# Kernel tuning notes

Hardware: AMD Instinct MI355X
Metric: run time of the kernel (lower is better)

The kernel has to match this reference:

```python
import jax, jax.numpy as jnp
import numpy as np
from jax import lax

Z_MAX = 0.3
WAVELENGTHS = jnp.array([0.65, 0.53, 0.47], jnp.float32)
LUMA = jnp.array([0.299, 0.587, 0.114], jnp.float32)


def conv2d(x, w, b):
    # x: (B,C,H,W), w: (O,I,kh,kw), SAME padding, stride 1
    y = lax.conv_general_dilated(x, w, (1, 1), 'SAME',
                                 dimension_numbers=('NCHW', 'OIHW', 'NCHW'))
    return y + b[None, :, None, None]


def group_norm(x, g, b, eps=1e-5):
    # GroupNorm(num_groups=1): normalize over (C,H,W) per sample
    mu = x.mean(axis=(1, 2, 3), keepdims=True)
    var = ((x - mu) ** 2).mean(axis=(1, 2, 3), keepdims=True)
    xn = (x - mu) * lax.rsqrt(var + eps)
    return xn * g[None, :, None, None] + b[None, :, None, None]


def setup_inputs() -> dict:
    key = jax.random.key(0)
    ks = jax.random.split(key, 16)
    B, C, H, W = 8, 3, 512, 512
    PH, ZH, MH = 16, 16, 32
    s = 0.1
    inp = {
        'x': jax.random.uniform(ks[0], (B, C, H, W), jnp.float32),
        'norm_g': jnp.ones((C,), jnp.float32), 'norm_b': jnp.zeros((C,), jnp.float32),
        'ph_w1': jax.random.normal(ks[1], (PH, C, 3, 3), jnp.float32) * s,
        'ph_b1': jnp.zeros((PH,), jnp.float32),
        'ph_w2': jax.random.normal(ks[2], (C, PH, 3, 3), jnp.float32) * s,
        'ph_b2': jnp.zeros((C,), jnp.float32),
        'z_w1': jax.random.normal(ks[3], (ZH, C, 3, 3), jnp.float32) * s,
        'z_b1': jnp.zeros((ZH,), jnp.float32),
        'z_w2': jax.random.normal(ks[4], (C, ZH, 3, 3), jnp.float32) * s,
        'z_b2': jnp.zeros((C,), jnp.float32),
        'freq_gain': jax.random.normal(ks[5], (C,), jnp.float32) * 0.01,
        'mix_w1': jax.random.normal(ks[6], (MH, C + 2, 3, 3), jnp.float32) * s,
        'mix_b1': jnp.zeros((MH,), jnp.float32),
        'gn1_g': jnp.ones((MH,), jnp.float32), 'gn1_b': jnp.zeros((MH,), jnp.float32),
        'mix_w2': jax.random.normal(ks[7], (MH, MH, 3, 3), jnp.float32) * s,
        'mix_b2': jnp.zeros((MH,), jnp.float32),
        'gn2_g': jnp.ones((MH,), jnp.float32), 'gn2_b': jnp.zeros((MH,), jnp.float32),
        'mix_w3': jax.random.normal(ks[8], (C, MH, 1, 1), jnp.float32) * s,
        'mix_b3': jnp.zeros((C,), jnp.float32),
        'se_w1': jax.random.normal(ks[9], (4, C), jnp.float32) * s,   # mid = max(3//4,4)=4
        'se_b1': jnp.zeros((4,), jnp.float32),
        'se_w2': jax.random.normal(ks[10], (C, 4), jnp.float32) * s,
        'se_b2': jnp.zeros((C,), jnp.float32),
        'alpha': jnp.asarray(0.3, jnp.float32),
    }
    return inp


def reference(x, norm_g, norm_b, ph_w1, ph_b1, ph_w2, ph_b2,
              z_w1, z_b1, z_w2, z_b2, freq_gain,
              mix_w1, mix_b1, gn1_g, gn1_b, mix_w2, mix_b2, gn2_g, gn2_b,
              mix_w3, mix_b3, se_w1, se_b1, se_w2, se_b2, alpha):
    B, C, H, W = x.shape
    # 1) norm
    xn = group_norm(x, norm_g, norm_b)
    # 2) phase prediction (small CNN, phi in [-pi, pi])
    h = jax.nn.silu(conv2d(xn, ph_w1, ph_b1))
    phi = jnp.tanh(conv2d(h, ph_w2, ph_b2)) * jnp.pi
    # 3) per-pixel propagation distance z in [0, z_max]
    hz = jax.nn.silu(conv2d(xn, z_w1, z_b1))
    z = jax.nn.sigmoid(conv2d(hz, z_w2, z_b2)) * Z_MAX
    # 4) complex field U0 = amp * exp(i*phi)  (amp_mode='identity')
    U0 = lax.complex(x * jnp.cos(phi), x * jnp.sin(phi))
    # 5) ASM propagation. kz = 2*pi*sqrt(1/lam^2 - fx^2 - fy^2), per-channel wavelength.
    fy = jnp.fft.fftfreq(H).astype(jnp.float32)
    fx = jnp.fft.fftfreq(W).astype(jnp.float32)
    f2 = fy[:, None] ** 2 + fx[None, :] ** 2                     # (H,W)
    inv_l2 = (1.0 / WAVELENGTHS ** 2)[:, None, None]             # (3,1,1)
    kz = 2.0 * jnp.pi * jnp.sqrt(jnp.maximum(inv_l2 - f2[None], 0.0))  # (3,H,W)
    # spatially varying z: base propagation at mean z + spatial phase correction
    z_mean = z.mean(axis=(2, 3), keepdims=True)                  # (B,3,1,1)
    Uf = jnp.fft.fft2(U0)
    Uf = Uf * (1.0 + freq_gain)[None, :, None, None].astype(Uf.dtype)  # FreqEnhance gain
    hp = kz[None] * z_mean                                       # (B,3,H,W)
    Uz = jnp.fft.ifft2(Uf * lax.complex(jnp.cos(hp), jnp.sin(hp)))
    k0 = (2.0 * jnp.pi / WAVELENGTHS)[None, :, None, None]
    cp = k0 * (z - z_mean)
    Uz = Uz * lax.complex(jnp.cos(cp), jnp.sin(cp))
    # 6) J = |Uz| with clamped sqrt
    J = jnp.sqrt(jnp.maximum(Uz.real ** 2 + Uz.imag ** 2, 1e-12))
    # 7) mix head: [x, J_luma, J_contrast] -> delta
    lw = LUMA[None, :, None, None]
    x_l = (x * lw).sum(axis=1, keepdims=True)
    J_l = (J * lw).sum(axis=1, keepdims=True)
    mix_in = jnp.concatenate([x, J_l, J_l - x_l], axis=1)        # (B,5,H,W)
    d = jax.nn.silu(group_norm(conv2d(mix_in, mix_w1, mix_b1), gn1_g, gn1_b))
    d = jax.nn.silu(group_norm(conv2d(d, mix_w2, mix_b2), gn2_g, gn2_b))
    delta = conv2d(d, mix_w3, mix_b3)                            # (B,3,H,W)
    # 8) SE channel attention
    p = delta.mean(axis=(2, 3))                                  # (B,3)
    wse = jax.nn.sigmoid(jax.nn.silu(p @ se_w1.T + se_b1) @ se_w2.T + se_b2)
    delta = delta * wse[:, :, None, None]
    # 9) residual update
    return x + alpha * delta
```

## Files before the change

kernel.cpp:

```cpp
#include <hip/hip_runtime.h>
#include <hip/hip_bf16.h>
#include <math.h>

#define DINL __device__ __forceinline__

namespace {
constexpr int Bn = 8, Cn = 3, Hn = 512, Wn = 512;
constexpr int HW  = Hn * Wn;
constexpr int CHW = Cn * HW;
constexpr float GEPS = 1e-5f;
constexpr float PIf  = 3.14159265358979323846f;

constexpr size_t OFF_RED = 0;
constexpr size_t OFF_PHI = 512;
constexpr size_t OFF_U   = OFF_PHI + (size_t)Bn * CHW * 2;
constexpr size_t OFF_J   = OFF_U   + (size_t)Bn * CHW * 4;
constexpr size_t OFF_D   = OFF_J   + (size_t)Bn * CHW * 2;
constexpr size_t OFF_Y2  = OFF_D   + (size_t)Bn * CHW * 2;
constexpr size_t OFF_W1B = OFF_Y2  + (size_t)Bn * 32 * HW;
constexpr size_t OFF_W2F = OFF_W1B + 3072 * 2;
constexpr size_t OFF_WH1 = OFF_W2F + 9216;
constexpr size_t OFF_WP2 = OFF_WH1 + 4608 * 2;
constexpr size_t OFF_WZ2 = OFF_WP2 + 4608;
constexpr size_t OFF_PRM = OFF_WZ2 + 4608;
constexpr size_t OFF_PART= OFF_PRM + 160 * 4;
constexpr int PZ = 0;
constexpr int PG1 = 24576;
constexpr int PG2 = 40960;
constexpr int PD  = 57344;
}

typedef __bf16 bfx8 __attribute__((ext_vector_type(8)));
typedef float  fx4  __attribute__((ext_vector_type(4)));
typedef float  fx2  __attribute__((ext_vector_type(2)));

DINL float frcp(float a) { return __builtin_amdgcn_rcpf(a); }
DINL float sigm(float a) { return frcp(1.f + __expf(-a)); }
DINL float siluf(float a) { return a * frcp(1.f + __expf(-a)); }
DINL float ftanh(float a) { return 1.f - 2.f * frcp(1.f + __expf(2.f * a)); }
DINL unsigned short f2bf(float f) {
    unsigned u = __float_as_uint(f);
    return (unsigned short)((u + 0x7FFFu + ((u >> 16) & 1u)) >> 16);
}
DINL float bf2f(unsigned short h) {
    return __uint_as_float(((unsigned)h) << 16);
}
DINL unsigned short t1(float a) { return (unsigned short)(__float_as_uint(a) >> 16); }
DINL unsigned t2(float a, float b) {
    return (__float_as_uint(a) >> 16) | (__float_as_uint(b) & 0xFFFF0000u);
}
DINL unsigned char f2f8(float v) {
    return (unsigned char)(__builtin_amdgcn_cvt_pk_fp8_f32(v, v, 0, false) & 0xFF);
}
DINL unsigned short pk8(float a, float b) {
    return (unsigned short)(__builtin_amdgcn_cvt_pk_fp8_f32(a, b, 0, false) & 0xFFFF);
}
DINL unsigned pk4f8(float a, float b, float c, float d) {
    unsigned u = __builtin_amdgcn_cvt_pk_fp8_f32(a, b, 0, false);
    u = __builtin_amdgcn_cvt_pk_fp8_f32(c, d, u, true);
    return u;
}
template<int SEL>
DINL float f8f(unsigned u) { return __builtin_amdgcn_cvt_f32_fp8(u, SEL); }
DINL unsigned pkh(float a, float b) {
    auto h = __builtin_amdgcn_cvt_pkrtz(a, b);
    unsigned u; __builtin_memcpy(&u, &h, 4); return u;
}
DINL float2 uph(unsigned u) {
    _Float16 h[2]; __builtin_memcpy(h, &u, 4);
    return make_float2((float)h[0], (float)h[1]);
}
DINL unsigned short f2h(float a) {
    _Float16 h = (_Float16)a; unsigned short s; __builtin_memcpy(&s, &h, 2); return s;
}
DINL float h2f(unsigned short s) {
    _Float16 h; __builtin_memcpy(&h, &s, 2); return (float)h;
}

DINL int SW(int e) { return e ^ ((e >> 4) & 7); }

DINL float blockReduceSum(float v) {
    __shared__ float sm[4];
    int lane = threadIdx.x & 63, wid = threadIdx.x >> 6;
    #pragma unroll
    for (int o = 32; o > 0; o >>= 1) v += __shfl_down(v, o, 64);
    __syncthreads();
    if (lane == 0) sm[wid] = v;
    __syncthreads();
    if (wid == 0) {
        float r = (lane < 4) ? sm[lane] : 0.f;
        r += __shfl_down(r, 2, 64);
        r += __shfl_down(r, 1, 64);
        return r;
    }
    return 0.f;
}

DINL void blockReduceSum3(float& a, float& b, float& c) {
    __shared__ float sm3[12];
    int lane = threadIdx.x & 63, wid = threadIdx.x >> 6;
    #pragma unroll
    for (int o = 32; o > 0; o >>= 1) {
        a += __shfl_down(a, o, 64);
        b += __shfl_down(b, o, 64);
        c += __shfl_down(c, o, 64);
    }
    __syncthreads();
    if (lane == 0) { sm3[wid] = a; sm3[4 + wid] = b; sm3[8 + wid] = c; }
    __syncthreads();
    if (threadIdx.x == 0) {
        a = sm3[0] + sm3[1] + sm3[2] + sm3[3];
        b = sm3[4] + sm3[5] + sm3[6] + sm3[7];
        c = sm3[8] + sm3[9] + sm3[10] + sm3[11];
    }
}

__global__ __launch_bounds__(256) void k_red(const float* __restrict__ src,
                                             float* __restrict__ dst)
{
    const float4* s4 = (const float4*)(src + (size_t)blockIdx.x * 1024);
    float4 q = s4[threadIdx.x];
    float r = blockReduceSum(q.x + q.y + q.z + q.w);
    if (threadIdx.x == 0) dst[blockIdx.x] = r;
}

__global__ __launch_bounds__(256) void k_init(
    const float* __restrict__ w1, const float* __restrict__ w2,
    const float* __restrict__ phw1, const float* __restrict__ zw1,
    const float* __restrict__ phw2, const float* __restrict__ zw2,
    const float* __restrict__ g2g, const float* __restrict__ g2b,
    const float* __restrict__ w3,
    unsigned short* __restrict__ w1bf, unsigned char* __restrict__ w2f8,
    unsigned short* __restrict__ wh1, unsigned char* __restrict__ wp2,
    unsigned char* __restrict__ wz2, float* __restrict__ prm,
    const float* __restrict__ x, float* __restrict__ part)
{
    if (blockIdx.x < 36) {
        int i = blockIdx.x * 256 + threadIdx.x;
        if (i < 3072) {
            int o = i / 96, k = i - o * 96;
            int ky = k >> 5, r = k & 31, kx = r >> 3, c = r & 7;
            float v = (kx < 3 && c < 5) ? w1[o * 45 + c * 9 + ky * 3 + kx] : 0.f;
            w1bf[i] = f2bf(v);
        }
        if (i < 9216) {
            int tap = i >> 10, rr = i & 1023, o = rr >> 5, ci = rr & 31;
            w2f8[i] = f2f8(w2[o * 288 + ci * 9 + tap]);
        }
        if (i < 4608) {
            int o = i / 96, k = i - o * 96;
            int ky = k >> 5, r = k & 31, kx = r >> 3, c = r & 7;
            float v = 0.f;
            if (kx < 3 && c < 3)
                v = (o < 16) ? phw1[o * 27 + c * 9 + ky * 3 + kx]
                             : zw1[(o - 16) * 27 + c * 9 + ky * 3 + kx];
            wh1[i] = f2bf(v);
        }
        if (i < 4608) {
            int tap = i / 512, rr = i - tap * 512, n = rr >> 5, k = rr & 31;
            float vp = (n < 3 && k < 16) ? phw2[n * 144 + k * 9 + tap] : 0.f;
            float vz = (n < 3) ? zw2[n * 288 + k * 9 + tap] : 0.f;
            wp2[i] = f2f8(vp);
            wz2[i] = f2f8(vz);
        }
        if (i < 160) {
            if (i < 32) {
                int ch = (i & 1) * 16 + (i >> 1);
                prm[i] = g2g[ch];
            } else if (i < 64) {
                int j = i - 32, ch = (j & 1) * 16 + (j >> 1);
                prm[i] = g2b[ch];
            } else {
                int j = (i - 64) & 31, c = (i - 64) >> 5;
                int ch = (j & 1) * 16 + (j >> 1);
                prm[i] = w3[c * 32 + ch];
            }
        }
        return;
    }
    const int bid = blockIdx.x - 36;
    const int b = bid >> 5, blk = bid & 31;
    const float4* xv = (const float4*)(x + (size_t)b * CHW + (size_t)blk * (CHW / 32));
    float s = 0.f, ss = 0.f;
    for (int i = threadIdx.x; i < (CHW / 32) / 4; i += 256) {
        float4 v = xv[i];
        s  += v.x + v.y + v.z + v.w;
        ss += v.x * v.x + v.y * v.y + v.z * v.z + v.w * v.w;
    }
    float rs = blockReduceSum(s);
    float rss = blockReduceSum(ss);
    if (threadIdx.x == 0) {
        part[PG1 + b * 64 + blk] = rs;
        part[PG1 + b * 64 + 32 + blk] = rss;
    }
}

__global__ __launch_bounds__(256) void k_heads(
    const float* __restrict__ x,
    const float* __restrict__ ng, const float* __restrict__ nb,
    const unsigned short* __restrict__ wh1,
    const float* __restrict__ phb1, const float* __restrict__ zb1,
    const unsigned char* __restrict__ wp2, const unsigned char* __restrict__ wz2,
    const float* __restrict__ phb2, const float* __restrict__ zb2,
    unsigned short* __restrict__ phi, float* __restrict__ part)
{
    const int tx0 = blockIdx.x * 16, ty0 = blockIdx.y * 16, b = blockIdx.z;
    const int local = blockIdx.y * 32 + blockIdx.x;
    const bool edge = (blockIdx.x == 0) || (blockIdx.x == 31) ||
                      (blockIdx.y == 0) || (blockIdx.y == 31);
    __shared__ unsigned short mt8[20 * 21 * 8];
    __shared__ __attribute__((aligned(16))) unsigned char ht8[324 * 48];
    __shared__ float xst[2];
    const int t = threadIdx.x;
    {
        const float* px = part + PG1 + (size_t)b * 64;
        float sv  = (t < 32) ? px[t] : 0.f;
        float ssv = (t >= 32 && t < 64) ? px[t] : 0.f;
        float r0 = blockReduceSum(sv);
        float r1 = blockReduceSum(ssv);
        if (t == 0) { xst[0] = r0; xst[1] = r1; }
        __syncthreads();
    }
    const float mu = xst[0] * (1.f / CHW);
    const float rsv = rsqrtf(xst[1] * (1.f / CHW) - mu * mu + GEPS);
    float sc[3], sh[3];
    #pragma unroll
    for (int c = 0; c < 3; ++c) { sc[c] = rsv * ng[c]; sh[c] = nb[c] - mu * rsv * ng[c]; }
    if (edge) {
        for (int e = t; e < 20 * 21; e += 256) {
            int yy = e / 21, xx = e - yy * 21;
            int gy = ty0 - 2 + yy, gx = tx0 - 2 + xx;
            float v0 = 0, v1 = 0, v2 = 0;
            if (xx < 20 && (unsigned)gy < (unsigned)Hn && (unsigned)gx < (unsigned)Wn) {
                size_t p = (size_t)b * CHW + (size_t)gy * Wn + gx;
                v0 = x[p] * sc[0] + sh[0];
                v1 = x[p + HW] * sc[1] + sh[1];
                v2 = x[p + 2 * HW] * sc[2] + sh[2];
            }
            *(uint4*)(mt8 + e * 8) = make_uint4(t2(v0, v1), (unsigned)t1(v2), 0u, 0u);
        }
    } else {
        for (int e = t; e < 20 * 21; e += 256) {
            int yy = e / 21, xx = e - yy * 21;
            float v0 = 0, v1 = 0, v2 = 0;
            if (xx < 20) {
                size_t p = (size_t)b * CHW + (size_t)(ty0 - 2 + yy) * Wn + (tx0 - 2 + xx);
                v0 = x[p] * sc[0] + sh[0];
                v1 = x[p + HW] * sc[1] + sh[1];
                v2 = x[p + 2 * HW] * sc[2] + sh[2];
            }
            *(uint4*)(mt8 + e * 8) = make_uint4(t2(v0, v1), (unsigned)t1(v2), 0u, 0u);
        }
    }
    const int wv = t >> 6, lane = t & 63, ln = lane & 15, q = lane >> 4;
    bfx8 Bf[3][3];
    #pragma unroll
    for (int ks = 0; ks < 3; ++ks)
        #pragma unroll
        for (int nt = 0; nt < 3; ++nt)
            Bf[ks][nt] = *(const bfx8*)(wh1 + (nt * 16 + ln) * 96 + ks * 32 + q * 8);
    float bph[4], bz0[4], bz1[4];
    #pragma unroll
    for (int r = 0; r < 4; ++r) {
        int ch = q * 4 + r;
        bph[r] = phb1[ch]; bz0[r] = zb1[ch]; bz1[r] = zb1[16 + ch];
    }
    __syncthreads();
    for (int mt = wv; mt < 21; mt += 4) {
        int p = mt * 16 + ln; if (p > 323) p = 323;
        const int hy = p / 18, hx = p - hy * 18;
        fx4 a0 = {0,0,0,0}, a1 = {0,0,0,0}, a2 = {0,0,0,0};
        #pragma unroll
        for (int ks = 0; ks < 3; ++ks) {
            bfx8 A = *(const bfx8*)(mt8 + ((hy + ks) * 21 + hx + q) * 8);
            a0 = __builtin_amdgcn_mfma_f32_16x16x32_bf16(Bf[ks][0], A, a0, 0, 0, 0);
            a1 = __builtin_amdgcn_mfma_f32_16x16x32_bf16(Bf[ks][1], A, a1, 0, 0, 0);
            a2 = __builtin_amdgcn_mfma_f32_16x16x32_bf16(Bf[ks][2], A, a2, 0, 0, 0);
        }
        bool live = true;
        if (edge) {
            const int gy = ty0 - 1 + hy, gx = tx0 - 1 + hx;
            live = (unsigned)gy < (unsigned)Hn && (unsigned)gx < (unsigned)Wn;
        }
        unsigned d0 = pk4f8(siluf(a0[0] + bph[0]), siluf(a0[1] + bph[1]),
                            siluf(a0[2] + bph[2]), siluf(a0[3] + bph[3]));
        unsigned d1 = pk4f8(siluf(a1[0] + bz0[0]), siluf(a1[1] + bz0[1]),
                            siluf(a1[2] + bz0[2]), siluf(a1[3] + bz0[3]));
        unsigned d2 = pk4f8(siluf(a2[0] + bz1[0]), siluf(a2[1] + bz1[1]),
                            siluf(a2[2] + bz1[2]), siluf(a2[3] + bz1[3]));
        if (!live) { d0 = 0u; d1 = 0u; d2 = 0u; }
        unsigned* hp = (unsigned*)(ht8 + p * 48 + q * 4);
        hp[0] = d0; hp[4] = d1; hp[8] = d2;
    }
    __syncthreads();
    fx4 accp[4], accz[4];
    #pragma unroll
    for (int i = 0; i < 4; ++i) { accp[i] = fx4{0,0,0,0}; accz[i] = fx4{0,0,0,0}; }
    #pragma unroll
    for (int tap = 0; tap < 9; ++tap) {
        const int ky = tap / 3, kx = tap - ky * 3;
        long Bp = *(const long*)(wp2 + tap * 512 + ln * 32 + q * 8);
        long Bz = *(const long*)(wz2 + tap * 512 + ln * 32 + q * 8);
        #pragma unroll
        for (int i = 0; i < 4; ++i) {
            const int oy = wv * 4 + i;
            const unsigned char* ap = ht8 + ((oy + ky) * 18 + ln + kx) * 48;
            long Ap = *(const long*)(ap + q * 8);
            long Az = *(const long*)(ap + 16 + q * 8);
            accp[i] = __builtin_amdgcn_mfma_f32_16x16x32_fp8_fp8(Ap, Bp, accp[i], 0, 0, 0);
            accz[i] = __builtin_amdgcn_mfma_f32_16x16x32_fp8_fp8(Az, Bz, accz[i], 0, 0, 0);
        }
    }
    __syncthreads();
    float* phs = (float*)ht8;
    float* zs  = phs + 1024;
    if (ln < 3) {
        #pragma unroll
        for (int i = 0; i < 4; ++i)
            #pragma unroll
            for (int r = 0; r < 4; ++r) {
                int pl = (wv * 4 + i) * 16 + q * 4 + r;
                phs[pl * 4 + ln] = accp[i][r];
                zs [pl * 4 + ln] = accz[i][r];
            }
    }
    asm volatile("" ::: "memory");
    float4 pv = ((const float4*)phs)[t];
    float4 zv = ((const float4*)zs)[t];
    const int gy = ty0 + (t >> 4), gx = tx0 + (t & 15);
    size_t pp = (size_t)b * CHW + (size_t)gy * Wn + gx;
    phi[pp]          = f2h(ftanh(pv.x + phb2[0]) * PIf);
    phi[pp + HW]     = f2h(ftanh(pv.y + phb2[1]) * PIf);
    phi[pp + 2 * HW] = f2h(ftanh(pv.z + phb2[2]) * PIf);
    float z0 = sigm(zv.x + zb2[0]) * 0.3f;
    float z1 = sigm(zv.y + zb2[1]) * 0.3f;
    float z2 = sigm(zv.z + zb2[2]) * 0.3f;
    blockReduceSum3(z0, z1, z2);
    if (t == 0) {
        part[PZ + (size_t)(b * 3 + 0) * 1024 + local] = z0;
        part[PZ + (size_t)(b * 3 + 1) * 1024 + local] = z1;
        part[PZ + (size_t)(b * 3 + 2) * 1024 + local] = z2;
    }
}

template<bool INV>
DINL float2* fft512_wave4(float2* a, float2* b, const float2* tw, int l)
{
    float2* src = a; float2* dst = b;
    int s = 1;
    #pragma unroll
    for (int st = 0; st < 4; ++st) {
        #pragma unroll
        for (int h = 0; h < 2; ++h) {
            const int i = l + h * 64;
            const int q = i & (s - 1);
            const int sm = i - q;
            const int si = SW(i);
            float2 A = src[si], B = src[si + 128], C = src[si + 256], D = src[si + 384];
            float t0x = A.x + C.x, t0y = A.y + C.y;
            float t1x = A.x - C.x, t1y = A.y - C.y;
            float t2x = B.x + D.x, t2y = B.y + D.y;
            float t3x = B.x - D.x, t3y = B.y - D.y;
            float i3x = INV ? -t3y : t3y;
            float i3y = INV ? t3x : -t3x;
            float u0x = t0x + t2x, u0y = t0y + t2y;
            float u2x = t0x - t2x, u2y = t0y - t2y;
            float u1x = t1x + i3x, u1y = t1y + i3y;
            float u3x = t1x - i3x, u3y = t1y - i3y;
            float2 w1 = tw[SW(sm)], w2 = tw[SW(2 * sm)], w3 = tw[SW(3 * sm)];
            float w1y = INV ? -w1.y : w1.y;
            float w2y = INV ? -w2.y : w2.y;
            float w3y = INV ? -w3.y : w3.y;
            const int base = q + 4 * sm;
            dst[SW(base)]         = make_float2(u0x, u0y);
            dst[SW(base + s)]     = make_float2(u1x * w1.x - u1y * w1y, u1x * w1y + u1y * w1.x);
            dst[SW(base + 2 * s)] = make_float2(u2x * w2.x - u2y * w2y, u2x * w2y + u2y * w2.x);
            dst[SW(base + 3 * s)] = make_float2(u3x * w3.x - u3y * w3y, u3x * w3y + u3y * w3.x);
        }
        float2* tmp = src; src = dst; dst = tmp;
        s <<= 2;
        asm volatile("" ::: "memory");
    }
    #pragma unroll
    for (int h = 0; h < 4; ++h) {
        const int j = l + h * 64;
        const int sj = SW(j);
        float2 u = src[sj], v = src[sj + 256];
        dst[sj]       = make_float2(u.x + v.x, u.y + v.y);
        dst[sj + 256] = make_float2(u.x - v.x, u.y - v.y);
    }
    float2* tmp = src; src = dst; dst = tmp;
    asm volatile("" ::: "memory");
    return src;
}

__global__ __launch_bounds__(256) void k_fftA(
    const float* __restrict__ x, const unsigned short* __restrict__ phi,
    unsigned* __restrict__ U)
{
    __shared__ float2 buf[4][2][512];
    __shared__ float2 tw[512];
    const int t = threadIdx.x, wv = t >> 6, l = t & 63;
    #pragma unroll
    for (int i = t; i < 512; i += 256) {
        float s, c; __sincosf(-2.f * PIf * (float)i * (1.f / 512.f), &s, &c);
        tw[SW(i)] = make_float2(c, s);
    }
    __syncthreads();
    const size_t line = (size_t)blockIdx.x * 4 + wv;
    const float* xr = x + line * 512;
    const unsigned short* pr = phi + line * 512;
    float2* A = buf[wv][0];
    float2* B = buf[wv][1];
    #pragma unroll
    for (int i = l; i < 512; i += 64) {
        float s, c; __sincosf(h2f(pr[i]), &s, &c);
        float xv = xr[i];
        A[SW(i)] = make_float2(xv * c, xv * s);
    }
    asm volatile("" ::: "memory");
    float2* res = fft512_wave4<false>(A, B, tw, l);
    unsigned* Ur = U + line * 512;
    #pragma unroll
    for (int i = l; i < 512; i += 64) {
        float2 v = res[SW(i)];
        Ur[i] = pkh(v.x, v.y);
    }
}

__global__ __launch_bounds__(256) void k_transpose(unsigned* __restrict__ U)
{
    const int img = blockIdx.y;
    int rem = blockIdx.x, ti = 0;
    while (rem >= 8 - ti) { rem -= 8 - ti; ++ti; }
    const int tj = ti + rem;
    unsigned* Ub = U + (size_t)img * HW;
    __shared__ unsigned ta[64][65];
    __shared__ unsigned tb[64][65];
    const int t = threadIdx.x;
    const int cc = t & 63, r0 = t >> 6;
    const int ar = ti * 64, ac = tj * 64;
    #pragma unroll
    for (int k = 0; k < 16; ++k) {
        int r = r0 + k * 4;
        ta[r][cc] = Ub[(size_t)(ar + r) * 512 + ac + cc];
    }
    if (ti != tj) {
        #pragma unroll
        for (int k = 0; k < 16; ++k) {
            int r = r0 + k * 4;
            tb[r][cc] = Ub[(size_t)(ac + r) * 512 + ar + cc];
        }
    }
    __syncthreads();
    #pragma unroll
    for (int k = 0; k < 16; ++k) {
        int r = r0 + k * 4;
        Ub[(size_t)(ac + r) * 512 + ar + cc] = ta[cc][r];
    }
    if (ti != tj) {
        #pragma unroll
        for (int k = 0; k < 16; ++k) {
            int r = r0 + k * 4;
            Ub[(size_t)(ar + r) * 512 + ac + cc] = tb[cc][r];
        }
    }
}

__global__ __launch_bounds__(256) void k_fftB(
    unsigned* __restrict__ U, const float* __restrict__ part, const float* __restrict__ fgain)
{
    __shared__ float2 buf[4][2][512];
    __shared__ float2 tw[512];
    __shared__ float zmS;
    const int t = threadIdx.x, wv = t >> 6, l = t & 63;
    #pragma unroll
    for (int i = t; i < 512; i += 256) {
        float s, c; __sincosf(-2.f * PIf * (float)i * (1.f / 512.f), &s, &c);
        tw[SW(i)] = make_float2(c, s);
    }
    const int bc0 = (blockIdx.x * 4) >> 9;
    {
        float4 a4 = ((const float4*)(part + PZ + (size_t)bc0 * 1024))[t];
        float r = blockReduceSum(a4.x + a4.y + a4.z + a4.w);
        if (t == 0) zmS = r * (1.f / HW);
    }
    __syncthreads();
    const int line = blockIdx.x * 4 + wv;
    const int bc = line >> 9;
    const int fw = line & 511;
    const int c = bc % 3;
    unsigned* Ur = U + (size_t)line * 512;
    float2* A = buf[wv][0];
    float2* B = buf[wv][1];
    #pragma unroll
    for (int i = l; i < 512; i += 64) A[SW(i)] = uph(Ur[i]);
    asm volatile("" ::: "memory");
    float2* res = fft512_wave4<false>(A, B, tw, l);
    const float zm   = zmS;
    const float gain = 1.f + fgain[c];
    const float lam  = (c == 0) ? 0.65f : (c == 1) ? 0.53f : 0.47f;
    const float il2  = 1.f / (lam * lam);
    const float fwv  = (float)(fw < 256 ? fw : fw - 512) * (1.f / 512.f);
    const float f2w  = fwv * fwv;
    #pragma unroll
    for (int i = l; i < 512; i += 64) {
        float fh = (float)(i < 256 ? i : i - 512) * (1.f / 512.f);
        float kz = 2.f * PIf * sqrtf(fmaxf(il2 - f2w - fh * fh, 0.f));
        float sn, cs; __sincosf(kz * zm, &sn, &cs);
        const int si = SW(i);
        float2 v = res[si];
        res[si] = make_float2(gain * (v.x * cs - v.y * sn), gain * (v.x * sn + v.y * cs));
    }
    asm volatile("" ::: "memory");
    float2* other = (res == A) ? B : A;
    float2* res2 = fft512_wave4<true>(res, other, tw, l);
    #pragma unroll
    for (int i = l; i < 512; i += 64) {
        float2 v = res2[SW(i)];
        Ur[i] = pkh(v.x * (1.f / 512.f), v.y * (1.f / 512.f));
    }
}

__global__ __launch_bounds__(256) void k_fftC(
    const unsigned* __restrict__ U, unsigned short* __restrict__ J)
{
    __shared__ float2 buf[4][2][512];
    __shared__ float2 tw[512];
    const int t = threadIdx.x, wv = t >> 6, l = t & 63;
    #pragma unroll
    for (int i = t; i < 512; i += 256) {
        float s, c; __sincosf(-2.f * PIf * (float)i * (1.f / 512.f), &s, &c);
        tw[SW(i)] = make_float2(c, s);
    }
    __syncthreads();
    const size_t line = (size_t)blockIdx.x * 4 + wv;
    const unsigned* Ur = U + line * 512;
    float2* A = buf[wv][0];
    float2* B = buf[wv][1];
    #pragma unroll
    for (int i = l; i < 512; i += 64) A[SW(i)] = uph(Ur[i]);
    asm volatile("" ::: "memory");
    float2* res = fft512_wave4<true>(A, B, tw, l);
    unsigned short* Jr = J + line * 512;
    #pragma unroll
    for (int i = l; i < 512; i += 64) {
        float2 v = res[SW(i)];
        float re = v.x * (1.f / 512.f), im = v.y * (1.f / 512.f);
        Jr[i] = f2h(sqrtf(fmaxf(re * re + im * im, 1e-12f)));
    }
}

__global__ __launch_bounds__(256) void k_m1(
    const float* __restrict__ x, const unsigned short* __restrict__ Jb,
    const unsigned short* __restrict__ w1bf, const float* __restrict__ b1,
    float* __restrict__ part)
{
    const int tx0 = blockIdx.x * 16, ty0 = blockIdx.y * 16, b = blockIdx.z;
    const int local = blockIdx.y * 32 + blockIdx.x;
    const bool edge = (blockIdx.x == 0) || (blockIdx.x == 31) ||
                      (blockIdx.y == 0) || (blockIdx.y == 31);
    __shared__ unsigned short mt8[18 * 19 * 8];
    const int t = threadIdx.x;
    for (int e = t; e < 18 * 19; e += 256) {
        int yy = e / 19, xx = e - yy * 19;
        int gy = ty0 - 1 + yy, gx = tx0 - 1 + xx;
        float v0 = 0, v1 = 0, v2 = 0, jl = 0, d5 = 0;
        bool ok = edge ? (xx < 18 && (unsigned)gy < (unsigned)Hn && (unsigned)gx < (unsigned)Wn)
                       : (xx < 18);
        if (ok) {
            size_t p = (size_t)b * CHW + (size_t)gy * Wn + gx;
            v0 = x[p]; v1 = x[p + HW]; v2 = x[p + 2 * HW];
            float j0 = h2f(Jb[p]), j1 = h2f(Jb[p + HW]), j2 = h2f(Jb[p + 2 * HW]);
            float xl = 0.299f * v0 + 0.587f * v1 + 0.114f * v2;
            jl = 0.299f * j0 + 0.587f * j1 + 0.114f * j2;
            d5 = jl - xl;
        }
        *(uint4*)(mt8 + e * 8) = make_uint4(t2(v0, v1), t2(v2, jl), (unsigned)t1(d5), 0u);
    }
    __syncthreads();
    const int wv = t >> 6, lane = t & 63, ln = lane & 15, q = lane >> 4;
    bfx8 Bf[3][2];
    #pragma unroll
    for (int ks = 0; ks < 3; ++ks)
        #pragma unroll
        for (int nt = 0; nt < 2; ++nt)
            Bf[ks][nt] = *(const bfx8*)(w1bf + (nt * 16 + ln) * 96 + ks * 32 + q * 8);
    const float b1v0 = b1[ln], b1v1 = b1[16 + ln];
    float s = 0.f, ss = 0.f;
    #pragma unroll
    for (int i = 0; i < 4; ++i) {
        const int oy = wv * 4 + i;
        fx4 a0 = {0.f, 0.f, 0.f, 0.f}, a1 = {0.f, 0.f, 0.f, 0.f};
        #pragma unroll
        for (int ks = 0; ks < 3; ++ks) {
            bfx8 A = *(const bfx8*)(mt8 + ((oy + ks) * 19 + ln + q) * 8);
            a0 = __builtin_amdgcn_mfma_f32_16x16x32_bf16(A, Bf[ks][0], a0, 0, 0, 0);
            a1 = __builtin_amdgcn_mfma_f32_16x16x32_bf16(A, Bf[ks][1], a1, 0, 0, 0);
        }
        #pragma unroll
        for (int r = 0; r < 4; ++r) {
            float u0 = a0[r] + b1v0, u1 = a1[r] + b1v1;
            s += u0 + u1; ss += u0 * u0 + u1 * u1;
        }
    }
    float rs = blockReduceSum(s);
    float rss = blockReduceSum(ss);
    if (t == 0) {
        part[PG1 + (size_t)b * 1024 + local] = rs;
        part[PG1 + (size_t)(8 + b) * 1024 + local] = rss;
    }
}

__global__ __launch_bounds__(256) void k_m2(
    const float* __restrict__ x, const unsigned short* __restrict__ Jb,
    const unsigned short* __restrict__ w1bf, const float* __restrict__ b1,
    const float* __restrict__ g1g, const float* __restrict__ g1b,
    const unsigned char* __restrict__ w2f8, const float* __restrict__ b2,
    float* __restrict__ part, unsigned char* __restrict__ y2)
{
    const int tx0 = blockIdx.x * 16, ty0 = blockIdx.y * 16, b = blockIdx.z;
    const int local = blockIdx.y * 32 + blockIdx.x;
    const bool edge = (blockIdx.x == 0) || (blockIdx.x == 31) ||
                      (blockIdx.y == 0) || (blockIdx.y == 31);
    __shared__ unsigned short mt8[20 * 21 * 8];
    __shared__ __attribute__((aligned(16))) unsigned char dt2[324 * 40];
    __shared__ float g1s[2];
    const int t = threadIdx.x;
    {
        float4 a4 = ((const float4*)(part + PG1 + (size_t)b * 1024))[t];
        float4 c4 = ((const float4*)(part + PG1 + (size_t)(8 + b) * 1024))[t];
        float r0 = blockReduceSum(a4.x + a4.y + a4.z + a4.w);
        float r1 = blockReduceSum(c4.x + c4.y + c4.z + c4.w);
        if (t == 0) { g1s[0] = r0; g1s[1] = r1; }
        __syncthreads();
    }
    const float mu1 = g1s[0] * (1.f / (32.f * HW));
    const float rs1 = rsqrtf(g1s[1] * (1.f / (32.f * HW)) - mu1 * mu1 + GEPS);
    for (int e = t; e < 20 * 21; e += 256) {
        int yy = e / 21, xx = e - yy * 21;
        int gy = ty0 - 2 + yy, gx = tx0 - 2 + xx;
        float v0 = 0, v1 = 0, v2 = 0, jl = 0, d5 = 0;
        bool ok = edge ? (xx < 20 && (unsigned)gy < (unsigned)Hn && (unsigned)gx < (unsigned)Wn)
                       : (xx < 20);
        if (ok) {
            size_t p = (size_t)b * CHW + (size_t)gy * Wn + gx;
            v0 = x[p]; v1 = x[p + HW]; v2 = x[p + 2 * HW];
            float j0 = h2f(Jb[p]), j1 = h2f(Jb[p + HW]), j2 = h2f(Jb[p + 2 * HW]);
            float xl = 0.299f * v0 + 0.587f * v1 + 0.114f * v2;
            jl = 0.299f * j0 + 0.587f * j1 + 0.114f * j2;
            d5 = jl - xl;
        }
        *(uint4*)(mt8 + e * 8) = make_uint4(t2(v0, v1), t2(v2, jl), (unsigned)t1(d5), 0u);
    }
    const int wv = t >> 6, lane = t & 63, ln = lane & 15, q = lane >> 4;
    float scv[2][4], ofv[2][4];
    #pragma unroll
    for (int g = 0; g < 2; ++g)
        #pragma unroll
        for (int r = 0; r < 4; ++r) {
            int ch = g * 16 + q * 4 + r;
            float sg = rs1 * g1g[ch];
            scv[g][r] = sg;
            ofv[g][r] = (b1[ch] - mu1) * sg + g1b[ch];
        }
    bfx8 Bf[3][2];
    #pragma unroll
    for (int ks = 0; ks < 3; ++ks)
        #pragma unroll
        for (int nt = 0; nt < 2; ++nt)
            Bf[ks][nt] = *(const bfx8*)(w1bf + (nt * 16 + ln) * 96 + ks * 32 + q * 8);
    __syncthreads();
    for (int mt = wv; mt < 21; mt += 4) {
        int p = mt * 16 + ln; if (p > 323) p = 323;
        const int hy = p / 18, hx = p - hy * 18;
        fx4 a0 = {0.f, 0.f, 0.f, 0.f}, a1 = {0.f, 0.f, 0.f, 0.f};
        #pragma unroll
        for (int ks = 0; ks < 3; ++ks) {
            bfx8 A = *(const bfx8*)(mt8 + ((hy + ks) * 21 + hx + q) * 8);
            a0 = __builtin_amdgcn_mfma_f32_16x16x32_bf16(Bf[ks][0], A, a0, 0, 0, 0);
            a1 = __builtin_amdgcn_mfma_f32_16x16x32_bf16(Bf[ks][1], A, a1, 0, 0, 0);
        }
        bool live = true;
        if (edge) {
            const int gy = ty0 - 1 + hy, gx = tx0 - 1 + hx;
            live = (unsigned)gy < (unsigned)Hn && (unsigned)gx < (unsigned)Wn;
        }
        unsigned d0 = pk4f8(siluf(a0[0] * scv[0][0] + ofv[0][0]),
                            siluf(a0[1] * scv[0][1] + ofv[0][1]),
                            siluf(a0[2] * scv[0][2] + ofv[0][2]),
                            siluf(a0[3] * scv[0][3] + ofv[0][3]));
        unsigned d1 = pk4f8(siluf(a1[0] * scv[1][0] + ofv[1][0]),
                            siluf(a1[1] * scv[1][1] + ofv[1][1]),
                            siluf(a1[2] * scv[1][2] + ofv[1][2]),
                            siluf(a1[3] * scv[1][3] + ofv[1][3]));
        if (!live) { d0 = 0u; d1 = 0u; }
        unsigned* dp = (unsigned*)(dt2 + p * 40 + q * 4);
        dp[0] = d0; dp[4] = d1;
    }
    __syncthreads();
    fx4 c2[4][2];
    #pragma unroll
    for (int i = 0; i < 4; ++i)
        #pragma unroll
        for (int nt = 0; nt < 2; ++nt)
            c2[i][nt] = fx4{0.f, 0.f, 0.f, 0.f};
    #pragma unroll
    for (int tap = 0; tap < 9; ++tap) {
        const int ky = tap / 3, kx = tap - ky * 3;
        long B0 = *(const long*)(w2f8 + tap * 1024 + ln * 32 + q * 8);
        long B1 = *(const long*)(w2f8 + tap * 1024 + (16 + ln) * 32 + q * 8);
        #pragma unroll
        for (int i = 0; i < 4; ++i) {
            const int oy = wv * 4 + i;
            long A = *(const long*)(dt2 + ((oy + ky) * 18 + ln + kx) * 40 + q * 8);
            c2[i][0] = __builtin_amdgcn_mfma_f32_16x16x32_fp8_fp8(A, B0, c2[i][0], 0, 0, 0);
            c2[i][1] = __builtin_amdgcn_mfma_f32_16x16x32_fp8_fp8(A, B1, c2[i][1], 0, 0, 0);
        }
    }
    float s = 0.f, ss = 0.f;
    const float b2v0 = b2[ln], b2v1 = b2[16 + ln];
    #pragma unroll
    for (int i = 0; i < 4; ++i) {
        const int gy = ty0 + wv * 4 + i;
        #pragma unroll
        for (int r = 0; r < 4; ++r) {
            const int gx = tx0 + q * 4 + r;
            float a0 = c2[i][0][r] + b2v0;
            float a1 = c2[i][1][r] + b2v1;
            s += a0 + a1; ss += a0 * a0 + a1 * a1;
            size_t off = ((size_t)b * HW + (size_t)gy * Wn + gx) * 32 + ln * 2;
            *(unsigned short*)(y2 + off) = pk8(a0, a1);
        }
    }
    float rsum = blockReduceSum(s);
    float rss = blockReduceSum(ss);
    if (t == 0) {
        part[PG2 + (size_t)b * 1024 + local] = rsum;
        part[PG2 + (size_t)(8 + b) * 1024 + local] = rss;
    }
}

__global__ __launch_bounds__(256) void k_m3(
    const unsigned char* __restrict__ y2,
    const float* __restrict__ prm, const float* __restrict__ b3,
    unsigned short* __restrict__ dl, float* __restrict__ part)
{
    const int t = threadIdx.x;
    const int b = blockIdx.x >> 10;
    __shared__ float g2s[2];
    {
        float4 a4 = ((const float4*)(part + PG2 + (size_t)b * 1024))[t];
        float4 c4 = ((const float4*)(part + PG2 + (size_t)(8 + b) * 1024))[t];
        float r0 = blockReduceSum(a4.x + a4.y + a4.z + a4.w);
        float r1 = blockReduceSum(c4.x + c4.y + c4.z + c4.w);
        if (t == 0) { g2s[0] = r0; g2s[1] = r1; }
        __syncthreads();
    }
    const float mu = g2s[0] * (1.f / (32.f * HW));
    const float rs = rsqrtf(g2s[1] * (1.f / (32.f * HW)) - mu * mu + GEPS);
    int idx = blockIdx.x * 256 + t;
    int pix = idx & (HW - 1);
    const int local = blockIdx.x & 1023;
    const uint4* yp = (const uint4*)(y2 + (size_t)idx * 32);
    uint4 L0 = yp[0], L1 = yp[1];
    unsigned Lw[8] = {L0.x, L0.y, L0.z, L0.w, L1.x, L1.y, L1.z, L1.w};
    float a0 = b3[0], a1 = b3[1], a2 = b3[2];
    #pragma unroll
    for (int w = 0; w < 8; ++w) {
        unsigned u = Lw[w];
#if __has_builtin(__builtin_amdgcn_cvt_pk_f32_fp8)
        fx2 lo = __builtin_amdgcn_cvt_pk_f32_fp8(u, false);
        fx2 hi = __builtin_amdgcn_cvt_pk_f32_fp8(u, true);
        float vv[4] = { lo[0], lo[1], hi[0], hi[1] };
#else
        float vv[4] = { f8f<0>(u), f8f<1>(u), f8f<2>(u), f8f<3>(u) };
#endif
        #pragma unroll
        for (int h = 0; h < 4; ++h) {
            int j = w * 4 + h;
            float dn = (vv[h] - mu) * rs * prm[j] + prm[32 + j];
            float sv = siluf(dn);
            a0 += sv * prm[64 + j]; a1 += sv * prm[96 + j]; a2 += sv * prm[128 + j];
        }
    }
    size_t p = (size_t)b * CHW + pix;
    dl[p] = f2h(a0); dl[p + HW] = f2h(a1); dl[p + 2 * HW] = f2h(a2);
    blockReduceSum3(a0, a1, a2);
    if (t == 0) {
        part[PD + (size_t)(b * 3 + 0) * 1024 + local] = a0;
        part[PD + (size_t)(b * 3 + 1) * 1024 + local] = a1;
        part[PD + (size_t)(b * 3 + 2) * 1024 + local] = a2;
    }
}

__global__ void k_se(float* __restrict__ red,
    const float* __restrict__ w1, const float* __restrict__ b1,
    const float* __restrict__ w2, const float* __restrict__ b2,
    const float* __restrict__ alpha)
{
    int b = threadIdx.x;
    if (b < 8) {
        float p0 = red[72 + b * 3 + 0] * (1.f / HW);
        float p1 = red[72 + b * 3 + 1] * (1.f / HW);
        float p2 = red[72 + b * 3 + 2] * (1.f / HW);
        float h[4];
        #pragma unroll
        for (int j = 0; j < 4; ++j) {
            float a = b1[j] + p0 * w1[j * 3] + p1 * w1[j * 3 + 1] + p2 * w1[j * 3 + 2];
            h[j] = siluf(a);
        }
        float al = alpha[0];
        #pragma unroll
        for (int c = 0; c < 3; ++c) {
            float a = b2[c] + h[0] * w2[c * 4] + h[1] * w2[c * 4 + 1]
                            + h[2] * w2[c * 4 + 2] + h[3] * w2[c * 4 + 3];
            red[96 + b * 3 + c] = al * sigm(a);
        }
    }
}

__global__ __launch_bounds__(256) void k_out(
    const float* __restrict__ x, const unsigned short* __restrict__ dl,
    const float* __restrict__ red, float* __restrict__ out)
{
    int i = blockIdx.x * 256 + threadIdx.x;
    float aw = red[96 + (i >> 16)];
    float4 xv = ((const float4*)x)[i];
    uint2 dv2 = ((const uint2*)dl)[i];
    float2 d01 = uph(dv2.x);
    float2 d23 = uph(dv2.y);
    float4 o;
    o.x = xv.x + aw * d01.x; o.y = xv.y + aw * d01.y;
    o.z = xv.z + aw * d23.x; o.w = xv.w + aw * d23.y;
    ((float4*)out)[i] = o;
}

extern "C" void kernel_launch(void* const* d_in, const int* in_sizes, int n_in,
                              void* d_out, int out_size, void* d_ws, size_t ws_size,
                              hipStream_t stream)
{
    const float* x     = (const float*)d_in[0];
    const float* ng    = (const float*)d_in[1];
    const float* nb    = (const float*)d_in[2];
    const float* ph_w1 = (const float*)d_in[3];
    const float* ph_b1 = (const float*)d_in[4];
    const float* ph_w2 = (const float*)d_in[5];
    const float* ph_b2 = (const float*)d_in[6];
    const float* z_w1  = (const float*)d_in[7];
    const float* z_b1  = (const float*)d_in[8];
    const float* z_w2  = (const float*)d_in[9];
    const float* z_b2  = (const float*)d_in[10];
    const float* fgain = (const float*)d_in[11];
    const float* mw1   = (const float*)d_in[12];
    const float* mb1   = (const float*)d_in[13];
    const float* g1g   = (const float*)d_in[14];
    const float* g1b   = (const float*)d_in[15];
    const float* mw2   = (const float*)d_in[16];
    const float* mb2   = (const float*)d_in[17];
    const float* g2g   = (const float*)d_in[18];
    const float* g2b   = (const float*)d_in[19];
    const float* mw3   = (const float*)d_in[20];
    const float* mb3   = (const float*)d_in[21];
    const float* sw1   = (const float*)d_in[22];
    const float* sb1   = (const float*)d_in[23];
    const float* sw2   = (const float*)d_in[24];
    const float* sb2   = (const float*)d_in[25];
    const float* alpha = (const float*)d_in[26];

    char* ws = (char*)d_ws;
    float*  red = (float*)(ws + OFF_RED);
    unsigned short* phi = (unsigned short*)(ws + OFF_PHI);
    unsigned* U = (unsigned*)(ws + OFF_U);
    unsigned short* Jb = (unsigned short*)(ws + OFF_J);
    unsigned short* dl = (unsigned short*)(ws + OFF_D);
    unsigned char*  y2   = (unsigned char*)(ws + OFF_Y2);
    unsigned short* w1bf = (unsigned short*)(ws + OFF_W1B);
    unsigned char*  w2f8 = (unsigned char*)(ws + OFF_W2F);
    unsigned short* wh1  = (unsigned short*)(ws + OFF_WH1);
    unsigned char*  wp2  = (unsigned char*)(ws + OFF_WP2);
    unsigned char*  wz2  = (unsigned char*)(ws + OFF_WZ2);
    float* prm  = (float*)(ws + OFF_PRM);
    float* part = (float*)(ws + OFF_PART);
    float* out = (float*)d_out;

    hipLaunchKernelGGL(k_init, dim3(292), dim3(256), 0, stream,
                       mw1, mw2, ph_w1, z_w1, ph_w2, z_w2, g2g, g2b, mw3,
                       w1bf, w2f8, wh1, wp2, wz2, prm, x, part);
    hipLaunchKernelGGL(k_heads, dim3(32, 32, 8), dim3(256), 0, stream,
                       x, ng, nb, wh1, ph_b1, z_b1, wp2, wz2, ph_b2, z_b2, phi, part);
    hipLaunchKernelGGL(k_fftA, dim3(3072), dim3(256), 0, stream, x, phi, U);
    hipLaunchKernelGGL(k_transpose, dim3(36, 24), dim3(256), 0, stream, U);
    hipLaunchKernelGGL(k_fftB, dim3(3072), dim3(256), 0, stream, U, part, fgain);
    hipLaunchKernelGGL(k_transpose, dim3(36, 24), dim3(256), 0, stream, U);
    hipLaunchKernelGGL(k_fftC, dim3(3072), dim3(256), 0, stream, U, Jb);
    hipLaunchKernelGGL(k_m1, dim3(32, 32, 8), dim3(256), 0, stream, x, Jb, w1bf, mb1, part);
    hipLaunchKernelGGL(k_m2, dim3(32, 32, 8), dim3(256), 0, stream,
                       x, Jb, w1bf, mb1, g1g, g1b, w2f8, mb2, part, y2);
    hipLaunchKernelGGL(k_m3, dim3(8192), dim3(256), 0, stream, y2, prm, mb3, dl, part);
    hipLaunchKernelGGL(k_red, dim3(24), dim3(256), 0, stream, part + PD, red + 72);
    hipLaunchKernelGGL(k_se, dim3(1), dim3(64), 0, stream, red, sw1, sb1, sw2, sb2, alpha);
    hipLaunchKernelGGL(k_out, dim3(6144), dim3(256), 0, stream, x, dl, red, out);
}
```

Before: 466.0 us.

## Precompute FFT twiddles, LUT-based GN2+SiLU in m3, merge final reductions

FFT twiddles are computed once in k_init into a global table, and the FFT kernels load them instead of calling sincos per block. The z-mean reduction moves from every k_fftB block into one transpose block per image. k_m3 now handles 2048 pixels per block and builds an 8192-entry shared-memory table of normalized SiLU values indexed by fp8 code, replacing per-element conversion and exp. k_red and k_se are merged into a single k_fin launch. The table build costs extra setup per block, and the larger blocks reduce parallelism in k_m3.

```diff
diff --git a/kernel.cpp b/kernel.cpp
--- a/kernel.cpp
+++ b/kernel.cpp
@@ -24,6 +24,7 @@
 constexpr size_t OFF_WZ2 = OFF_WP2 + 4608;
 constexpr size_t OFF_PRM = OFF_WZ2 + 4608;
 constexpr size_t OFF_PART= OFF_PRM + 160 * 4;
+constexpr size_t OFF_TW  = OFF_PART + 81920 * 4;
 constexpr int PZ = 0;
 constexpr int PG1 = 24576;
 constexpr int PG2 = 40960;
@@ -113,15 +114,6 @@
         b = sm3[4] + sm3[5] + sm3[6] + sm3[7];
         c = sm3[8] + sm3[9] + sm3[10] + sm3[11];
     }
-}
-
-__global__ __launch_bounds__(256) void k_red(const float* __restrict__ src,
-                                             float* __restrict__ dst)
-{
-    const float4* s4 = (const float4*)(src + (size_t)blockIdx.x * 1024);
-    float4 q = s4[threadIdx.x];
-    float r = blockReduceSum(q.x + q.y + q.z + q.w);
-    if (threadIdx.x == 0) dst[blockIdx.x] = r;
 }
 
 __global__ __launch_bounds__(256) void k_init(
@@ -133,6 +125,7 @@
     unsigned short* __restrict__ w1bf, unsigned char* __restrict__ w2f8,
     unsigned short* __restrict__ wh1, unsigned char* __restrict__ wp2,
     unsigned char* __restrict__ wz2, float* __restrict__ prm,
+    float2* __restrict__ gtw,
     const float* __restrict__ x, float* __restrict__ part)
 {
     if (blockIdx.x < 36) {
@@ -178,7 +171,14 @@
         }
         return;
     }
-    const int bid = blockIdx.x - 36;
+    if (blockIdx.x == 36) {
+        for (int i = threadIdx.x; i < 512; i += 256) {
+            float s, c; __sincosf(-2.f * PIf * (float)i * (1.f / 512.f), &s, &c);
+            gtw[i] = make_float2(c, s);
+        }
+        return;
+    }
+    const int bid = blockIdx.x - 37;
     const int b = bid >> 5, blk = bid & 31;
     const float4* xv = (const float4*)(x + (size_t)b * CHW + (size_t)blk * (CHW / 32));
     float s = 0.f, ss = 0.f;
@@ -396,16 +396,13 @@
 
 __global__ __launch_bounds__(256) void k_fftA(
     const float* __restrict__ x, const unsigned short* __restrict__ phi,
-    unsigned* __restrict__ U)
+    unsigned* __restrict__ U, const float2* __restrict__ gtw)
 {
     __shared__ float2 buf[4][2][512];
     __shared__ float2 tw[512];
     const int t = threadIdx.x, wv = t >> 6, l = t & 63;
     #pragma unroll
-    for (int i = t; i < 512; i += 256) {
-        float s, c; __sincosf(-2.f * PIf * (float)i * (1.f / 512.f), &s, &c);
-        tw[SW(i)] = make_float2(c, s);
-    }
+    for (int i = t; i < 512; i += 256) tw[SW(i)] = gtw[i];
     __syncthreads();
     const size_t line = (size_t)blockIdx.x * 4 + wv;
     const float* xr = x + line * 512;
@@ -428,9 +425,16 @@
     }
 }
 
-__global__ __launch_bounds__(256) void k_transpose(unsigned* __restrict__ U)
+__global__ __launch_bounds__(256) void k_transpose(unsigned* __restrict__ U,
+                                                   const float* __restrict__ part,
+                                                   float* __restrict__ red)
 {
     const int img = blockIdx.y;
+    if (blockIdx.x == 0) {
+        float4 a4 = ((const float4*)(part + PZ + (size_t)img * 1024))[threadIdx.x];
+        float r = blockReduceSum(a4.x + a4.y + a4.z + a4.w);
+        if (threadIdx.x == 0) red[16 + img] = r;
+    }
     int rem = blockIdx.x, ti = 0;
     while (rem >= 8 - ti) { rem -= 8 - ti; ++ti; }
     const int tj = ti + rem;
@@ -468,28 +472,20 @@
 }
 
 __global__ __launch_bounds__(256) void k_fftB(
-    unsigned* __restrict__ U, const float* __restrict__ part, const float* __restrict__ fgain)
+    unsigned* __restrict__ U, const float* __restrict__ red,
+    const float* __restrict__ fgain, const float2* __restrict__ gtw)
 {
     __shared__ float2 buf[4][2][512];
     __shared__ float2 tw[512];
-    __shared__ float zmS;
     const int t = threadIdx.x, wv = t >> 6, l = t & 63;
     #pragma unroll
-    for (int i = t; i < 512; i += 256) {
-        float s, c; __sincosf(-2.f * PIf * (float)i * (1.f / 512.f), &s, &c);
-        tw[SW(i)] = make_float2(c, s);
-    }
-    const int bc0 = (blockIdx.x * 4) >> 9;
-    {
-        float4 a4 = ((const float4*)(part + PZ + (size_t)bc0 * 1024))[t];
-        float r = blockReduceSum(a4.x + a4.y + a4.z + a4.w);
-        if (t == 0) zmS = r * (1.f / HW);
-    }
-    __syncthreads();
+    for (int i = t; i < 512; i += 256) tw[SW(i)] = gtw[i];
     const int line = blockIdx.x * 4 + wv;
     const int bc = line >> 9;
     const int fw = line & 511;
     const int c = bc % 3;
+    const float zm = red[16 + bc] * (1.f / HW);
+    __syncthreads();
     unsigned* Ur = U + (size_t)line * 512;
     float2* A = buf[wv][0];
     float2* B = buf[wv][1];
@@ -497,7 +493,6 @@
     for (int i = l; i < 512; i += 64) A[SW(i)] = uph(Ur[i]);
     asm volatile("" ::: "memory");
     float2* res = fft512_wave4<false>(A, B, tw, l);
-    const float zm   = zmS;
     const float gain = 1.f + fgain[c];
     const float lam  = (c == 0) ? 0.65f : (c == 1) ? 0.53f : 0.47f;
     const float il2  = 1.f / (lam * lam);
@@ -523,16 +518,14 @@
 }
 
 __global__ __launch_bounds__(256) void k_fftC(
-    const unsigned* __restrict__ U, unsigned short* __restrict__ J)
+    const unsigned* __restrict__ U, unsigned short* __restrict__ J,
+    const float2* __restrict__ gtw)
 {
     __shared__ float2 buf[4][2][512];
     __shared__ float2 tw[512];
     const int t = threadIdx.x, wv = t >> 6, l = t & 63;
     #pragma unroll
-    for (int i = t; i < 512; i += 256) {
-        float s, c; __sincosf(-2.f * PIf * (float)i * (1.f / 512.f), &s, &c);
-        tw[SW(i)] = make_float2(c, s);
-    }
+    for (int i = t; i < 512; i += 256) tw[SW(i)] = gtw[i];
     __syncthreads();
     const size_t line = (size_t)blockIdx.x * 4 + wv;
     const unsigned* Ur = U + line * 512;
@@ -747,8 +740,10 @@
     unsigned short* __restrict__ dl, float* __restrict__ part)
 {
     const int t = threadIdx.x;
-    const int b = blockIdx.x >> 10;
+    const int b = blockIdx.x >> 7;
+    const int local = blockIdx.x & 127;
     __shared__ float g2s[2];
+    __shared__ float lut[8192];
     {
         float4 a4 = ((const float4*)(part + PG2 + (size_t)b * 1024))[t];
         float4 c4 = ((const float4*)(part + PG2 + (size_t)(8 + b) * 1024))[t];
@@ -759,51 +754,66 @@
     }
     const float mu = g2s[0] * (1.f / (32.f * HW));
     const float rs = rsqrtf(g2s[1] * (1.f / (32.f * HW)) - mu * mu + GEPS);
-    int idx = blockIdx.x * 256 + t;
-    int pix = idx & (HW - 1);
-    const int local = blockIdx.x & 1023;
-    const uint4* yp = (const uint4*)(y2 + (size_t)idx * 32);
-    uint4 L0 = yp[0], L1 = yp[1];
-    unsigned Lw[8] = {L0.x, L0.y, L0.z, L0.w, L1.x, L1.y, L1.z, L1.w};
-    float a0 = b3[0], a1 = b3[1], a2 = b3[2];
-    #pragma unroll
-    for (int w = 0; w < 8; ++w) {
-        unsigned u = Lw[w];
-#if __has_builtin(__builtin_amdgcn_cvt_pk_f32_fp8)
-        fx2 lo = __builtin_amdgcn_cvt_pk_f32_fp8(u, false);
-        fx2 hi = __builtin_amdgcn_cvt_pk_f32_fp8(u, true);
-        float vv[4] = { lo[0], lo[1], hi[0], hi[1] };
-#else
-        float vv[4] = { f8f<0>(u), f8f<1>(u), f8f<2>(u), f8f<3>(u) };
-#endif
-        #pragma unroll
-        for (int h = 0; h < 4; ++h) {
-            int j = w * 4 + h;
-            float dn = (vv[h] - mu) * rs * prm[j] + prm[32 + j];
-            float sv = siluf(dn);
-            a0 += sv * prm[64 + j]; a1 += sv * prm[96 + j]; a2 += sv * prm[128 + j];
-        }
-    }
-    size_t p = (size_t)b * CHW + pix;
-    dl[p] = f2h(a0); dl[p + HW] = f2h(a1); dl[p + 2 * HW] = f2h(a2);
-    blockReduceSum3(a0, a1, a2);
+    for (int e = t; e < 8192; e += 256) {
+        int j = e >> 8;
+        float v = f8f<0>((unsigned)(e & 255));
+        lut[e] = siluf((v - mu) * rs * prm[j] + prm[32 + j]);
+    }
+    __syncthreads();
+    const float bb0 = b3[0], bb1 = b3[1], bb2 = b3[2];
+    float s0 = 0.f, s1 = 0.f, s2 = 0.f;
+    #pragma unroll
+    for (int k = 0; k < 8; ++k) {
+        int idx = blockIdx.x * 2048 + k * 256 + t;
+        int pix = idx & (HW - 1);
+        const uint4* yp = (const uint4*)(y2 + (size_t)idx * 32);
+        uint4 L0 = yp[0], L1 = yp[1];
+        unsigned Lw[8] = {L0.x, L0.y, L0.z, L0.w, L1.x, L1.y, L1.z, L1.w};
+        float a0 = bb0, a1 = bb1, a2 = bb2;
+        #pragma unroll
+        for (int w = 0; w < 8; ++w) {
+            unsigned u = Lw[w];
+            #pragma unroll
+            for (int h = 0; h < 4; ++h) {
+                int j = w * 4 + h;
+                int code = (int)((u >> (8 * h)) & 255u);
+                float sv = lut[j * 256 + code];
+                a0 += sv * prm[64 + j]; a1 += sv * prm[96 + j]; a2 += sv * prm[128 + j];
+            }
+        }
+        size_t p = (size_t)b * CHW + pix;
+        dl[p] = f2h(a0); dl[p + HW] = f2h(a1); dl[p + 2 * HW] = f2h(a2);
+        s0 += a0; s1 += a1; s2 += a2;
+    }
+    blockReduceSum3(s0, s1, s2);
     if (t == 0) {
-        part[PD + (size_t)(b * 3 + 0) * 1024 + local] = a0;
-        part[PD + (size_t)(b * 3 + 1) * 1024 + local] = a1;
-        part[PD + (size_t)(b * 3 + 2) * 1024 + local] = a2;
-    }
-}
-
-__global__ void k_se(float* __restrict__ red,
+        part[PD + (size_t)(b * 3 + 0) * 1024 + local] = s0;
+        part[PD + (size_t)(b * 3 + 1) * 1024 + local] = s1;
+        part[PD + (size_t)(b * 3 + 2) * 1024 + local] = s2;
+    }
+}
+
+__global__ __launch_bounds__(256) void k_fin(
+    const float* __restrict__ part, float* __restrict__ red,
     const float* __restrict__ w1, const float* __restrict__ b1,
     const float* __restrict__ w2, const float* __restrict__ b2,
     const float* __restrict__ alpha)
 {
-    int b = threadIdx.x;
-    if (b < 8) {
-        float p0 = red[72 + b * 3 + 0] * (1.f / HW);
-        float p1 = red[72 + b * 3 + 1] * (1.f / HW);
-        float p2 = red[72 + b * 3 + 2] * (1.f / HW);
+    __shared__ float sm[24];
+    const int t = threadIdx.x, wv = t >> 6, l = t & 63;
+    for (int g = wv; g < 24; g += 4) {
+        const float* p = part + PD + (size_t)g * 1024;
+        float s = p[l] + p[l + 64];
+        #pragma unroll
+        for (int o = 32; o > 0; o >>= 1) s += __shfl_down(s, o, 64);
+        if (l == 0) sm[g] = s;
+    }
+    __syncthreads();
+    if (t < 8) {
+        int b = t;
+        float p0 = sm[b * 3 + 0] * (1.f / HW);
+        float p1 = sm[b * 3 + 1] * (1.f / HW);
+        float p2 = sm[b * 3 + 2] * (1.f / HW);
         float h[4];
         #pragma unroll
         for (int j = 0; j < 4; ++j) {
@@ -882,23 +892,23 @@
     unsigned char*  wz2  = (unsigned char*)(ws + OFF_WZ2);
     float* prm  = (float*)(ws + OFF_PRM);
     float* part = (float*)(ws + OFF_PART);
+    float2* gtw = (float2*)(ws + OFF_TW);
     float* out = (float*)d_out;
 
-    hipLaunchKernelGGL(k_init, dim3(292), dim3(256), 0, stream,
+    hipLaunchKernelGGL(k_init, dim3(293), dim3(256), 0, stream,
                        mw1, mw2, ph_w1, z_w1, ph_w2, z_w2, g2g, g2b, mw3,
-                       w1bf, w2f8, wh1, wp2, wz2, prm, x, part);
+                       w1bf, w2f8, wh1, wp2, wz2, prm, gtw, x, part);
     hipLaunchKernelGGL(k_heads, dim3(32, 32, 8), dim3(256), 0, stream,
                        x, ng, nb, wh1, ph_b1, z_b1, wp2, wz2, ph_b2, z_b2, phi, part);
-    hipLaunchKernelGGL(k_fftA, dim3(3072), dim3(256), 0, stream, x, phi, U);
-    hipLaunchKernelGGL(k_transpose, dim3(36, 24), dim3(256), 0, stream, U);
-    hipLaunchKernelGGL(k_fftB, dim3(3072), dim3(256), 0, stream, U, part, fgain);
-    hipLaunchKernelGGL(k_transpose, dim3(36, 24), dim3(256), 0, stream, U);
-    hipLaunchKernelGGL(k_fftC, dim3(3072), dim3(256), 0, stream, U, Jb);
+    hipLaunchKernelGGL(k_fftA, dim3(3072), dim3(256), 0, stream, x, phi, U, gtw);
+    hipLaunchKernelGGL(k_transpose, dim3(36, 24), dim3(256), 0, stream, U, part, red);
+    hipLaunchKernelGGL(k_fftB, dim3(3072), dim3(256), 0, stream, U, red, fgain, gtw);
+    hipLaunchKernelGGL(k_transpose, dim3(36, 24), dim3(256), 0, stream, U, part, red);
+    hipLaunchKernelGGL(k_fftC, dim3(3072), dim3(256), 0, stream, U, Jb, gtw);
     hipLaunchKernelGGL(k_m1, dim3(32, 32, 8), dim3(256), 0, stream, x, Jb, w1bf, mb1, part);
     hipLaunchKernelGGL(k_m2, dim3(32, 32, 8), dim3(256), 0, stream,
                        x, Jb, w1bf, mb1, g1g, g1b, w2f8, mb2, part, y2);
-    hipLaunchKernelGGL(k_m3, dim3(8192), dim3(256), 0, stream, y2, prm, mb3, dl, part);
-    hipLaunchKernelGGL(k_red, dim3(24), dim3(256), 0, stream, part + PD, red + 72);
-    hipLaunchKernelGGL(k_se, dim3(1), dim3(64), 0, stream, red, sw1, sb1, sw2, sb2, alpha);
+    hipLaunchKernelGGL(k_m3, dim3(1024), dim3(256), 0, stream, y2, prm, mb3, dl, part);
+    hipLaunchKernelGGL(k_fin, dim3(1), dim3(256), 0, stream, part, red, sw1, sb1, sw2, sb2, alpha);
     hipLaunchKernelGGL(k_out, dim3(6144), dim3(256), 0, stream, x, dl, red, out);
 }
```

Measured after the change: 462.1 us. No clear change (-0.8%).
